# Kernel optimization log

Hardware: AMD Instinct MI355X
Metric: run time of the kernel (lower is better)

The kernel has to match this reference:

```python
import jax, jax.numpy as jnp
from jax import lax
import numpy as np

N_TIMESTEPS = 100000


def setup_inputs() -> dict:
    key = jax.random.key(0)
    k1, k2 = jax.random.split(key)
    params = jax.random.normal(k1, (11,), dtype=jnp.float32)
    epsilons = jax.random.normal(k2, (N_TIMESTEPS,), dtype=jnp.float32)
    return {"params": params, "epsilons": epsilons}


def reference(params, epsilons):
    # params: [log_beta, g1..g4, b1..b4, log_sigma, log_r]
    beta = jnp.exp(params[0])
    g = params[1:5]          # (4,)
    b = params[5:9]          # (4,)
    sigma = jnp.exp(params[-2])
    r = jnp.exp(params[-1])
    R = 1.0 + r

    # Faithful to the torch code: at step t (with x = hstack(zeros(3), x_0..x_{t-1})),
    # x[t-1], x[t-2], x[t-3] resolve to x_{t-4}, x_{t-5}, x_{t-6} (zeros for t<4/5/6;
    # the t=0 negative-index case also yields zeros, so a zero-initialized lag buffer
    # reproduces it exactly). Carry = (x_{t-6}, x_{t-5}, x_{t-4}, x_{t-3}, x_{t-2}, x_{t-1}).
    def step(carry, eps_t):
        xm6 = carry[0]
        xm5 = carry[1]
        xm4 = carry[2]
        exponent = beta * (xm4 - R * xm5) * (g * xm6 + b - R * xm5)  # (4,)
        w = jax.nn.softmax(exponent, axis=-1)                         # (4,)
        mean = jnp.sum(w * (g * xm4 + b))
        x_t = (mean + eps_t * sigma) / R
        new_carry = jnp.concatenate([carry[1:], x_t[None]])
        return new_carry, x_t

    init = jnp.zeros(6, dtype=params.dtype)
    _, xs = lax.scan(step, init, epsilons)
    return xs  # shape (n_timesteps,), equals x[3:] of the torch module
```

## Files before the change

kernel.cpp:

```cpp
#include <hip/hip_runtime.h>
#include <math.h>


constexpr int NT = 100000;
constexpr int NS = NT / 4;
constexpr int BURN_CHUNK  = 32768;
constexpr int BURN_CHUNKS = 60;

#define QPERM_XOR1 0xB1
#define QPERM_XOR2 0x4E
#define ROW_SHR4   0x114
#define ROW_SHR8   0x118
#define ROW_SHL8   0x108
#define ROW_SHL12  0x10C

template <int CTRL>
__device__ __forceinline__ float dppf(float x) {
    return __int_as_float(
        __builtin_amdgcn_update_dpp(0, __float_as_int(x), CTRL, 0xf, 0xf, true));
}

__global__ __launch_bounds__(256) void bh_wave(const float* __restrict__ params,
                                               const float* __restrict__ eps,
                                               float* __restrict__ out,
                                               int* __restrict__ flag) {
    if (blockIdx.x != 0) {
        float a = 1.0f + (float)threadIdx.x;
        float c = 0.9999f;
        float a2 = 2.0f;
        for (int ch = 0; ch < BURN_CHUNKS; ++ch) {
            for (int i = 0; i < BURN_CHUNK; ++i) {
                a  = __builtin_fmaf(a,  c, 1.0e-4f);
                a2 = __builtin_fmaf(a2, c, 2.0e-4f);
            }
            if (__hip_atomic_load(flag, __ATOMIC_RELAXED,
                                  __HIP_MEMORY_SCOPE_AGENT)) break;
        }
        asm volatile("" :: "v"(a), "v"(a2));
        return;
    }

    const int tid = threadIdx.x;

    if (tid >= 64) {
        float acc = 0.f;
        const float4* e4p = reinterpret_cast<const float4*>(eps);
        for (int i = tid - 64; i < NT / 4; i += 192) {
            float4 v = e4p[i];
            acc += v.x + v.y + v.z + v.w;
        }
        asm volatile("" :: "v"(acc));
        return;
    }
    if (tid >= 16) return;

    if (tid == 0) {
        __hip_atomic_store(flag, 0, __ATOMIC_RELAXED, __HIP_MEMORY_SCOPE_AGENT);
    }

    const int q = tid >> 2;
    const int j = tid & 3;

    const float beta   = expf(params[0]);
    const float g      = params[1 + j];
    const float b      = params[5 + j];
    const float sigma  = expf(params[9]);
    const float R      = 1.0f + expf(params[10]);
    const float Rinv   = 1.0f / R;
    const float beta2  = beta * 1.4426950408889634f;
    const float A2     = beta2 * Rinv;
    const float nbeta2 = -beta2;
    const float gR     = g * Rinv;

    float z  = 0.f;
    float zp = 0.f;

    float e0 = eps[4 * 0 + q], e1 = eps[4 * 1 + q];
    float e2 = eps[4 * 2 + q], e3 = eps[4 * 3 + q];
    float e4 = eps[4 * 4 + q], e5 = eps[4 * 5 + q];
    float e6 = eps[4 * 6 + q], e7 = eps[4 * 7 + q];

#define STEP(EV, SS)                                                          \
    {                                                                         \
        float bA  = A2 * z;                     \
        float vv  = __builtin_fmaf(gR, z, b);                                 \
        float ep2 = (EV) * sigma;                                             \
        float xm5 = dppf<ROW_SHR4>(z) + dppf<ROW_SHL12>(zp);                  \
        float xm6 = dppf<ROW_SHR8>(z) + dppf<ROW_SHL8>(zp);                   \
        float u   = __builtin_fmaf(gR, xm6, b);                               \
        float p   = __builtin_fmaf(nbeta2, xm5, bA);                          \
        float qq  = u - xm5;                                                  \
        float x   = p * qq;                                                   \
        float t   = __builtin_amdgcn_exp2f(x);                                \
        float tv  = t * vv;                                                   \
        float ts  = t  + dppf<QPERM_XOR1>(t);                                 \
        float tvs = tv + dppf<QPERM_XOR1>(tv);                                \
        ts  += dppf<QPERM_XOR2>(ts);                                          \
        tvs += dppf<QPERM_XOR2>(tvs);                                         \
        float rc   = __builtin_amdgcn_rcpf(ts);                               \
        float ynew = __builtin_fmaf(tvs, rc, ep2);                            \
        out[4 * (SS) + q] = ynew * Rinv;                 \
        zp = z; z = ynew;                                                     \
    }

    for (int s = 0; s < NS - 8; s += 8) {
        const int bse = s + 8;
        float n0 = eps[4 * (bse + 0) + q], n1 = eps[4 * (bse + 1) + q];
        float n2 = eps[4 * (bse + 2) + q], n3 = eps[4 * (bse + 3) + q];
        float n4 = eps[4 * (bse + 4) + q], n5 = eps[4 * (bse + 5) + q];
        float n6 = eps[4 * (bse + 6) + q], n7 = eps[4 * (bse + 7) + q];

        STEP(e0, s + 0);
        STEP(e1, s + 1);
        STEP(e2, s + 2);
        STEP(e3, s + 3);
        STEP(e4, s + 4);
        STEP(e5, s + 5);
        STEP(e6, s + 6);
        STEP(e7, s + 7);

        e0 = n0; e1 = n1; e2 = n2; e3 = n3;
        e4 = n4; e5 = n5; e6 = n6; e7 = n7;
    }
    {
        const int s = NS - 8;
        STEP(e0, s + 0);
        STEP(e1, s + 1);
        STEP(e2, s + 2);
        STEP(e3, s + 3);
        STEP(e4, s + 4);
        STEP(e5, s + 5);
        STEP(e6, s + 6);
        STEP(e7, s + 7);
    }
#undef STEP

    if (tid == 0) {
        __hip_atomic_store(flag, 1, __ATOMIC_RELAXED, __HIP_MEMORY_SCOPE_AGENT);
    }
}

extern "C" void kernel_launch(void* const* d_in, const int* in_sizes, int n_in,
                              void* d_out, int out_size, void* d_ws, size_t ws_size,
                              hipStream_t stream) {
    const float* params = (const float*)d_in[0];
    const float* eps    = (const float*)d_in[1];
    float*       out    = (float*)d_out;
    int*         flag   = (int*)d_ws;
    bh_wave<<<256, 256, 0, stream>>>(params, eps, out, flag);
}
```

Baseline: 1.561 ms.

## Prescale eps in helper waves and defer Rinv output scaling to post-pass

```diff
diff --git a/kernel.cpp b/kernel.cpp
--- a/kernel.cpp
+++ b/kernel.cpp
@@ -4,6 +4,7 @@
 
 constexpr int NT = 100000;
 constexpr int NS = NT / 4;
+constexpr int SW = 8192;
 constexpr int BURN_CHUNK  = 32768;
 constexpr int BURN_CHUNKS = 60;
 
@@ -23,7 +24,9 @@
 __global__ __launch_bounds__(256) void bh_wave(const float* __restrict__ params,
                                                const float* __restrict__ eps,
                                                float* __restrict__ out,
-                                               int* __restrict__ flag) {
+                                               int* __restrict__ flag,
+                                               float* __restrict__ wse,
+                                               int use_ws) {
     if (blockIdx.x != 0) {
         float a = 1.0f + (float)threadIdx.x;
         float c = 0.9999f;
@@ -43,18 +46,48 @@
     const int tid = threadIdx.x;
 
     if (tid >= 64) {
-        float acc = 0.f;
-        const float4* e4p = reinterpret_cast<const float4*>(eps);
-        for (int i = tid - 64; i < NT / 4; i += 192) {
-            float4 v = e4p[i];
-            acc += v.x + v.y + v.z + v.w;
-        }
-        asm volatile("" :: "v"(acc));
+        const float sigma = expf(params[9]);
+        const float Rinv  = 1.0f / (1.0f + expf(params[10]));
+        if (use_ws) {
+            const int lane = tid - 64;
+            const float4* e4p = reinterpret_cast<const float4*>(eps);
+            float4*       w4p = reinterpret_cast<float4*>(wse);
+            for (int i = lane; i < NT / 4; i += 192) {
+                float4 v = e4p[i];
+                v.x *= sigma; v.y *= sigma; v.z *= sigma; v.w *= sigma;
+                w4p[i] = v;
+            }
+            if (tid == 64) {
+                __hip_atomic_store(flag + 2, 1, __ATOMIC_RELEASE,
+                                   __HIP_MEMORY_SCOPE_WORKGROUP);
+            }
+            while (!__hip_atomic_load(flag + 1, __ATOMIC_ACQUIRE,
+                                      __HIP_MEMORY_SCOPE_WORKGROUP)) {
+                __builtin_amdgcn_s_sleep(8);
+            }
+            const int lane2 = tid - 64;
+            float4* o4p = reinterpret_cast<float4*>(out);
+            for (int i = lane2; i < NT / 4; i += 192) {
+                float4 v = o4p[i];
+                v.x *= Rinv; v.y *= Rinv; v.z *= Rinv; v.w *= Rinv;
+                o4p[i] = v;
+            }
+        } else {
+            float acc = 0.f;
+            const float4* e4p = reinterpret_cast<const float4*>(eps);
+            for (int i = tid - 64; i < NT / 4; i += 192) {
+                float4 v = e4p[i];
+                acc += v.x + v.y + v.z + v.w;
+            }
+            asm volatile("" :: "v"(acc));
+        }
         return;
     }
     if (tid >= 16) return;
 
     if (tid == 0) {
+        __hip_atomic_store(flag + 1, 0, __ATOMIC_RELAXED,
+                           __HIP_MEMORY_SCOPE_WORKGROUP);
         __hip_atomic_store(flag, 0, __ATOMIC_RELAXED, __HIP_MEMORY_SCOPE_AGENT);
     }
 
@@ -75,16 +108,15 @@
     float z  = 0.f;
     float zp = 0.f;
 
-    float e0 = eps[4 * 0 + q], e1 = eps[4 * 1 + q];
-    float e2 = eps[4 * 2 + q], e3 = eps[4 * 3 + q];
-    float e4 = eps[4 * 4 + q], e5 = eps[4 * 5 + q];
-    float e6 = eps[4 * 6 + q], e7 = eps[4 * 7 + q];
+    float e0 = eps[4 * 0 + q] * sigma, e1 = eps[4 * 1 + q] * sigma;
+    float e2 = eps[4 * 2 + q] * sigma, e3 = eps[4 * 3 + q] * sigma;
+    float e4 = eps[4 * 4 + q] * sigma, e5 = eps[4 * 5 + q] * sigma;
+    float e6 = eps[4 * 6 + q] * sigma, e7 = eps[4 * 7 + q] * sigma;
 
 #define STEP(EV, SS)                                                          \
     {                                                                         \
-        float bA  = A2 * z;                     \
+        float bA  = A2 * z;                                                   \
         float vv  = __builtin_fmaf(gR, z, b);                                 \
-        float ep2 = (EV) * sigma;                                             \
         float xm5 = dppf<ROW_SHR4>(z) + dppf<ROW_SHL12>(zp);                  \
         float xm6 = dppf<ROW_SHR8>(z) + dppf<ROW_SHL8>(zp);                   \
         float u   = __builtin_fmaf(gR, xm6, b);                               \
@@ -98,44 +130,72 @@
         ts  += dppf<QPERM_XOR2>(ts);                                          \
         tvs += dppf<QPERM_XOR2>(tvs);                                         \
         float rc   = __builtin_amdgcn_rcpf(ts);                               \
-        float ynew = __builtin_fmaf(tvs, rc, ep2);                            \
-        out[4 * (SS) + q] = ynew * Rinv;                 \
+        float ynew = __builtin_fmaf(tvs, rc, (EV));                           \
+        out[4 * (SS) + q] = ynew;              \
         zp = z; z = ynew;                                                     \
     }
 
-    for (int s = 0; s < NS - 8; s += 8) {
-        const int bse = s + 8;
-        float n0 = eps[4 * (bse + 0) + q], n1 = eps[4 * (bse + 1) + q];
-        float n2 = eps[4 * (bse + 2) + q], n3 = eps[4 * (bse + 3) + q];
-        float n4 = eps[4 * (bse + 4) + q], n5 = eps[4 * (bse + 5) + q];
-        float n6 = eps[4 * (bse + 6) + q], n7 = eps[4 * (bse + 7) + q];
-
-        STEP(e0, s + 0);
-        STEP(e1, s + 1);
-        STEP(e2, s + 2);
-        STEP(e3, s + 3);
-        STEP(e4, s + 4);
-        STEP(e5, s + 5);
-        STEP(e6, s + 6);
-        STEP(e7, s + 7);
-
-        e0 = n0; e1 = n1; e2 = n2; e3 = n3;
+#define PF_RAW(BSE)                                                           \
+        float n0 = eps[4 * ((BSE) + 0) + q] * sigma;                          \
+        float n1 = eps[4 * ((BSE) + 1) + q] * sigma;                          \
+        float n2 = eps[4 * ((BSE) + 2) + q] * sigma;                          \
+        float n3 = eps[4 * ((BSE) + 3) + q] * sigma;                          \
+        float n4 = eps[4 * ((BSE) + 4) + q] * sigma;                          \
+        float n5 = eps[4 * ((BSE) + 5) + q] * sigma;                          \
+        float n6 = eps[4 * ((BSE) + 6) + q] * sigma;                          \
+        float n7 = eps[4 * ((BSE) + 7) + q] * sigma;
+
+#define PF_WS(BSE)                                                            \
+        float n0 = wse[4 * ((BSE) + 0) + q];                                  \
+        float n1 = wse[4 * ((BSE) + 1) + q];                                  \
+        float n2 = wse[4 * ((BSE) + 2) + q];                                  \
+        float n3 = wse[4 * ((BSE) + 3) + q];                                  \
+        float n4 = wse[4 * ((BSE) + 4) + q];                                  \
+        float n5 = wse[4 * ((BSE) + 5) + q];                                  \
+        float n6 = wse[4 * ((BSE) + 6) + q];                                  \
+        float n7 = wse[4 * ((BSE) + 7) + q];
+
+#define BODY8(SBASE)                                                          \
+        STEP(e0, (SBASE) + 0); STEP(e1, (SBASE) + 1);                         \
+        STEP(e2, (SBASE) + 2); STEP(e3, (SBASE) + 3);                         \
+        STEP(e4, (SBASE) + 4); STEP(e5, (SBASE) + 5);                         \
+        STEP(e6, (SBASE) + 6); STEP(e7, (SBASE) + 7);                         \
+        e0 = n0; e1 = n1; e2 = n2; e3 = n3;                                   \
         e4 = n4; e5 = n5; e6 = n6; e7 = n7;
+
+    for (int s = 0; s < SW; s += 8) {
+        PF_RAW(s + 8)
+        BODY8(s)
+    }
+
+    const bool ws_ready = use_ws &&
+        __hip_atomic_load(flag + 2, __ATOMIC_ACQUIRE,
+                          __HIP_MEMORY_SCOPE_WORKGROUP);
+
+    if (ws_ready) {
+        for (int s = SW; s < NS - 8; s += 8) {
+            PF_WS(s + 8)
+            BODY8(s)
+        }
+    } else {
+        for (int s = SW; s < NS - 8; s += 8) {
+            PF_RAW(s + 8)
+            BODY8(s)
+        }
     }
     {
         const int s = NS - 8;
-        STEP(e0, s + 0);
-        STEP(e1, s + 1);
-        STEP(e2, s + 2);
-        STEP(e3, s + 3);
-        STEP(e4, s + 4);
-        STEP(e5, s + 5);
-        STEP(e6, s + 6);
-        STEP(e7, s + 7);
-    }
+        STEP(e0, s + 0); STEP(e1, s + 1); STEP(e2, s + 2); STEP(e3, s + 3);
+        STEP(e4, s + 4); STEP(e5, s + 5); STEP(e6, s + 6); STEP(e7, s + 7);
+    }
+#undef BODY8
+#undef PF_WS
+#undef PF_RAW
 #undef STEP
 
     if (tid == 0) {
+        __hip_atomic_store(flag + 1, 1, __ATOMIC_RELEASE,
+                           __HIP_MEMORY_SCOPE_WORKGROUP);
         __hip_atomic_store(flag, 1, __ATOMIC_RELAXED, __HIP_MEMORY_SCOPE_AGENT);
     }
 }
@@ -147,5 +207,7 @@
     const float* eps    = (const float*)d_in[1];
     float*       out    = (float*)d_out;
     int*         flag   = (int*)d_ws;
-    bh_wave<<<256, 256, 0, stream>>>(params, eps, out, flag);
+    float*       wse    = (float*)((char*)d_ws + 16);
+    const int    use_ws = (ws_size >= 16 + (size_t)NT * sizeof(float)) ? 1 : 0;
+    bh_wave<<<256, 256, 0, stream>>>(params, eps, out, flag, wse, use_ws);
 }
```

Result: faster. 1.421 ms (median of 2 runs) (-9.0%).
